# Kernel optimization log

Measured on AMD Instinct MI355X. Metric: run time of the kernel, lower is better.

## Reference

```python
import jax, jax.numpy as jnp
import numpy as np

B, T, H, LATENT, COND = 256, 256, 512, 64, 6
IN0 = 3 + H + 4  # lstm layer-0 input size


def _ln(x, g, b, eps=1e-5):
    m = x.mean(-1, keepdims=True)
    v = ((x - m) ** 2).mean(-1, keepdims=True)
    return (x - m) / jnp.sqrt(v + eps) * g + b


def setup_inputs() -> dict:
    key = jax.random.key(0)
    ks = jax.random.split(key, 24)
    p = lambda k, shape: (jax.random.normal(k, shape) * 0.02).astype(jnp.float32)
    inp = {
        'start': jax.random.uniform(ks[0], (B, 2), dtype=jnp.float32),
        'end': jax.random.uniform(ks[1], (B, 2), dtype=jnp.float32),
        'z': jax.random.normal(ks[2], (B, LATENT), dtype=jnp.float32),
        # condition encoder: Linear(6+latent->H), LN, Linear(H->H), LN
        'ce_w1': p(ks[3], (H, COND + LATENT)), 'ce_b1': jnp.zeros((H,), jnp.float32),
        'ce_g1': jnp.ones((H,), jnp.float32), 'ce_be1': jnp.zeros((H,), jnp.float32),
        'ce_w2': p(ks[4], (H, H)), 'ce_b2': jnp.zeros((H,), jnp.float32),
        'ce_g2': jnp.ones((H,), jnp.float32), 'ce_be2': jnp.zeros((H,), jnp.float32),
        # 2-layer LSTM (torch gate order i,f,g,o)
        'Wih0': p(ks[5], (4 * H, IN0)), 'Whh0': p(ks[6], (4 * H, H)),
        'bih0': jnp.zeros((4 * H,), jnp.float32), 'bhh0': jnp.zeros((4 * H,), jnp.float32),
        'Wih1': p(ks[7], (4 * H, H)), 'Whh1': p(ks[8], (4 * H, H)),
        'bih1': jnp.zeros((4 * H,), jnp.float32), 'bhh1': jnp.zeros((4 * H,), jnp.float32),
        # output head: Linear(H->H//2), LeakyReLU, Linear(H//2->3)
        'ow1': p(ks[9], (H // 2, H)), 'ob1': jnp.zeros((H // 2,), jnp.float32),
        'ow2': p(ks[10], (3, H // 2)), 'ob2': jnp.zeros((3,), jnp.float32),
        'init_in': jnp.zeros((1, 1, 3), jnp.float32),
        'max_len': T,
    }
    return inp


def _cell(x, h, c, Wih, Whh, bih, bhh):
    g = x @ Wih.T + bih + h @ Whh.T + bhh
    i, f, gg, o = jnp.split(g, 4, axis=-1)
    c2 = jax.nn.sigmoid(f) * c + jax.nn.sigmoid(i) * jnp.tanh(gg)
    h2 = jax.nn.sigmoid(o) * jnp.tanh(c2)
    return h2, c2


def reference(start, end, z, ce_w1, ce_b1, ce_g1, ce_be1, ce_w2, ce_b2, ce_g2, ce_be2,
              Wih0, Whh0, bih0, bhh0, Wih1, Whh1, bih1, bhh1,
              ow1, ob1, ow2, ob2, init_in, max_len):
    b = start.shape[0]
    hd = Whh0.shape[1]
    # condition vector
    diff = end - start
    dist = jnp.sqrt((diff ** 2).sum(-1, keepdims=True) + 1e-8)
    ang = jnp.arctan2(diff[:, 1:2], diff[:, 0:1])
    ci = jnp.concatenate([start, end, dist, ang, z], axis=-1)
    x = jax.nn.leaky_relu(_ln(ci @ ce_w1.T + ce_b1, ce_g1, ce_be1), 0.2)
    cond = jax.nn.leaky_relu(_ln(x @ ce_w2.T + ce_b2, ce_g2, ce_be2), 0.2)

    h0 = jnp.zeros((2, b, hd), start.dtype)
    c0 = jnp.zeros((2, b, hd), start.dtype)
    cur_in0 = jnp.broadcast_to(init_in.reshape(1, 3), (b, 3))

    def step(carry, _):
        h, c, cur_in, pos = carry
        rem = end - pos
        rd = jnp.sqrt((rem ** 2).sum(-1, keepdims=True) + 1e-8)
        ra = jnp.arctan2(rem[:, 1:2], rem[:, 0:1])
        xin = jnp.concatenate([cur_in, cond, rem, rd, ra], axis=-1)  # (B, 3+H+4)
        h1, c1 = _cell(xin, h[0], c[0], Wih0, Whh0, bih0, bhh0)
        h2, c2 = _cell(h1, h[1], c[1], Wih1, Whh1, bih1, bhh1)
        o = jax.nn.leaky_relu(h2 @ ow1.T + ob1, 0.2) @ ow2.T + ob2  # (B, 3)
        out = jnp.concatenate([o[:, :2], jax.nn.softplus(o[:, 2:3]) + 0.001], axis=-1)
        pos = pos + out[:, :2]
        return (jnp.stack([h1, h2]), jnp.stack([c1, c2]), out, pos), out

    _, outs = jax.lax.scan(step, (h0, c0, cur_in0, start), None, length=max_len)
    outputs = jnp.transpose(outs, (1, 0, 2))  # (B, T, 3)
    lengths = jnp.full((b,), max_len, dtype=jnp.int32)
    return outputs, lengths
```

## Files before the change

kernel.cpp:

```cpp
#include <hip/hip_runtime.h>
#include <math.h>

#define BB 256
#define TT 256
#define HH 512
#define G4 2048
#define IN0_ 519

typedef __bf16 bf16x8 __attribute__((ext_vector_type(8)));
typedef float  f32x4  __attribute__((ext_vector_type(4)));

__device__ __forceinline__ float sigf(float x) { return 1.0f / (1.0f + expf(-x)); }
__device__ __forceinline__ float leaky(float x) { return x > 0.f ? x : 0.2f * x; }

__device__ __forceinline__ unsigned short f2b(float x) {
    union { float f; unsigned int u; } v; v.f = x;
    unsigned int r = v.u + 0x7fffu + ((v.u >> 16) & 1u);
    return (unsigned short)(r >> 16);
}

__device__ __forceinline__ float block_sum(float v, float* red, int tid) {
    red[tid] = v; __syncthreads();
    for (int s = 128; s > 0; s >>= 1) {
        if (tid < s) red[tid] += red[tid + s];
        __syncthreads();
    }
    float r = red[0];
    __syncthreads();
    return r;
}

__global__ __launch_bounds__(256) void prep_weights(
    const float* __restrict__ Whh0, const float* __restrict__ Wih1,
    const float* __restrict__ Whh1, const float* __restrict__ Wih0,
    unsigned short* __restrict__ w0b, unsigned short* __restrict__ w1b,
    unsigned short* __restrict__ w2b, float* __restrict__ Wf)
{
    int idx = blockIdx.x * 256 + threadIdx.x;
    if (idx < G4 * HH) {
        w0b[idx] = f2b(Whh0[idx]);
        w1b[idx] = f2b(Wih1[idx]);
        w2b[idx] = f2b(Whh1[idx]);
    }
    if (idx < G4) {
        const int fc[7] = {0, 1, 2, 515, 516, 517, 518};
        #pragma unroll
        for (int f = 0; f < 7; f++) Wf[idx*8 + f] = Wih0[(size_t)idx*IN0_ + fc[f]];
        Wf[idx*8 + 7] = 0.f;
    }
}

__global__ void init_kernel(const float* __restrict__ start,
                            const float* __restrict__ init_in,
                            const int* __restrict__ max_len,
                            float* __restrict__ c0, float* __restrict__ c1,
                            unsigned short* __restrict__ h0u, unsigned short* __restrict__ h1u,
                            float* __restrict__ pos, float* __restrict__ cur,
                            float* __restrict__ out_tail)
{
    int i = blockIdx.x * blockDim.x + threadIdx.x;
    if (i < BB * HH) { c0[i] = 0.f; c1[i] = 0.f; h0u[i] = 0; h1u[i] = 0; }
    if (i < BB * 2) pos[i] = start[i];
    if (i < BB * 3) cur[i] = init_in[i % 3];
    if (i < BB)     out_tail[i] = (float)max_len[0];
}

__global__ __launch_bounds__(256) void cond_encoder(
    const float* __restrict__ start, const float* __restrict__ end,
    const float* __restrict__ z,
    const float* __restrict__ w1, const float* __restrict__ b1,
    const float* __restrict__ g1, const float* __restrict__ be1,
    const float* __restrict__ w2, const float* __restrict__ b2,
    const float* __restrict__ g2, const float* __restrict__ be2,
    float* __restrict__ cond)
{
    __shared__ float ci[70];
    __shared__ float xr[512];
    __shared__ float red[256];
    int b = blockIdx.x, tid = threadIdx.x;
    if (tid == 0) {
        float sx = start[2*b], sy = start[2*b+1];
        float ex = end[2*b],   ey = end[2*b+1];
        float dx = ex - sx, dy = ey - sy;
        ci[0]=sx; ci[1]=sy; ci[2]=ex; ci[3]=ey;
        ci[4]=sqrtf(dx*dx + dy*dy + 1e-8f);
        ci[5]=atan2f(dy, dx);
    }
    if (tid < 64) ci[6+tid] = z[b*64 + tid];
    __syncthreads();

    float pre0 = b1[tid], pre1 = b1[tid+256];
    {
        const float* r0 = w1 + (size_t)tid*70;
        const float* r1 = w1 + (size_t)(tid+256)*70;
        for (int k = 0; k < 70; k++) { float c = ci[k]; pre0 += c*r0[k]; pre1 += c*r1[k]; }
    }
    float m = block_sum(pre0+pre1, red, tid) * (1.f/512.f);
    float d0 = pre0-m, d1 = pre1-m;
    float v = block_sum(d0*d0 + d1*d1, red, tid) * (1.f/512.f);
    float rstd = rsqrtf(v + 1e-5f);
    xr[tid]     = leaky(d0*rstd*g1[tid]     + be1[tid]);
    xr[tid+256] = leaky(d1*rstd*g1[tid+256] + be1[tid+256]);
    __syncthreads();

    float q0 = b2[tid], q1 = b2[tid+256];
    {
        const float4* r0 = (const float4*)(w2 + (size_t)tid*512);
        const float4* r1 = (const float4*)(w2 + (size_t)(tid+256)*512);
        const float4* xv4 = (const float4*)xr;
        for (int q = 0; q < 128; q++) {
            float4 xv = xv4[q];
            float4 wa = r0[q], wb = r1[q];
            q0 += xv.x*wa.x + xv.y*wa.y + xv.z*wa.z + xv.w*wa.w;
            q1 += xv.x*wb.x + xv.y*wb.y + xv.z*wb.z + xv.w*wb.w;
        }
    }
    m = block_sum(q0+q1, red, tid) * (1.f/512.f);
    d0 = q0-m; d1 = q1-m;
    v = block_sum(d0*d0 + d1*d1, red, tid) * (1.f/512.f);
    rstd = rsqrtf(v + 1e-5f);
    cond[(size_t)b*512 + tid]     = leaky(d0*rstd*g2[tid]     + be2[tid]);
    cond[(size_t)b*512 + tid+256] = leaky(d1*rstd*g2[tid+256] + be2[tid+256]);
}

__global__ __launch_bounds__(256) void static_gates(
    const float* __restrict__ cond, const float* __restrict__ Wih0,
    const float* __restrict__ bih0, const float* __restrict__ bhh0,
    float* __restrict__ gs0)
{
    __shared__ float As[16][17];
    __shared__ float Bs[16][17];
    int tx = threadIdx.x & 15, ty = threadIdx.x >> 4;
    int brow = blockIdx.x * 16;
    int jcol = blockIdx.y * 16;
    float acc = 0.f;
    for (int kt = 0; kt < 512; kt += 16) {
        As[ty][tx] = cond[(size_t)(brow+ty)*512 + kt + tx];
        Bs[ty][tx] = Wih0[(size_t)(jcol+ty)*IN0_ + 3 + kt + tx];
        __syncthreads();
        #pragma unroll
        for (int kk = 0; kk < 16; kk++) acc += As[ty][kk] * Bs[tx][kk];
        __syncthreads();
    }
    int jg = jcol + tx;
    gs0[(size_t)(brow+ty)*G4 + jg] = acc + bih0[jg] + bhh0[jg];
}

__global__ __launch_bounds__(256) void lstm0_mfma(
    const unsigned short* __restrict__ Wb,
    const float* __restrict__ gs0,
    const float* __restrict__ Wf,
    const float* __restrict__ end, const float* __restrict__ pos,
    const float* __restrict__ cur,
    const unsigned short* __restrict__ h_in,
    const float* __restrict__ c_in,
    float* __restrict__ c_out,
    unsigned short* __restrict__ h_out)
{
    __shared__ float ct[4][16][16];
    __shared__ float feats[16][8];
    int tid = threadIdx.x;
    int w = tid >> 6, l = tid & 63;
    int lr = l & 15, lk = l >> 4;
    int m0 = blockIdx.x * 16;
    int n0 = blockIdx.y * 16;
    if (tid < 16) {
        int b = m0 + tid;
        float px = pos[2*b], py = pos[2*b+1];
        float ex = end[2*b], ey = end[2*b+1];
        float rx = ex - px, ry = ey - py;
        feats[tid][0] = cur[3*b];
        feats[tid][1] = cur[3*b+1];
        feats[tid][2] = cur[3*b+2];
        feats[tid][3] = rx;
        feats[tid][4] = ry;
        feats[tid][5] = sqrtf(rx*rx + ry*ry + 1e-8f);
        feats[tid][6] = atan2f(ry, rx);
        feats[tid][7] = 0.f;
    }
    int jg = w*512 + n0 + lr;
    f32x4 acc;
    #pragma unroll
    for (int r = 0; r < 4; r++)
        acc[r] = gs0[(size_t)(m0 + lk*4 + r)*G4 + jg];
    const unsigned short* ap = h_in + (size_t)(m0 + lr)*HH + lk*8;
    const unsigned short* bp = Wb   + (size_t)jg*HH + lk*8;
    #pragma unroll
    for (int kt = 0; kt < 16; kt++) {
        bf16x8 a = *reinterpret_cast<const bf16x8*>(ap + kt*32);
        bf16x8 b = *reinterpret_cast<const bf16x8*>(bp + kt*32);
        acc = __builtin_amdgcn_mfma_f32_16x16x32_bf16(a, b, acc, 0, 0, 0);
    }
    #pragma unroll
    for (int r = 0; r < 4; r++) ct[w][lk*4 + r][lr] = acc[r];
    __syncthreads();

    int bl = tid >> 4, jl = tid & 15;
    int b = m0 + bl;
    int j = n0 + jl;
    float g4[4];
    #pragma unroll
    for (int g = 0; g < 4; g++) {
        float v = ct[g][bl][jl];
        const float* wf = Wf + (size_t)(g*HH + j)*8;
        #pragma unroll
        for (int f = 0; f < 7; f++) v += feats[bl][f] * wf[f];
        g4[g] = v;
    }
    float ig = sigf(g4[0]), fg = sigf(g4[1]);
    float gg = tanhf(g4[2]), og = sigf(g4[3]);
    float cn = fg * c_in[(size_t)b*HH + j] + ig * gg;
    c_out[(size_t)b*HH + j] = cn;
    h_out[(size_t)b*HH + j] = f2b(og * tanhf(cn));
}

__global__ __launch_bounds__(256) void lstm1_mfma(
    const unsigned short* __restrict__ Wi,
    const unsigned short* __restrict__ Wh,
    const float* __restrict__ bi, const float* __restrict__ bh,
    const unsigned short* __restrict__ x,
    const unsigned short* __restrict__ h_in,
    const float* __restrict__ c_in,
    float* __restrict__ c_out,
    unsigned short* __restrict__ h_out, float* __restrict__ h_out_f)
{
    __shared__ float ct[4][16][16];
    int tid = threadIdx.x;
    int w = tid >> 6, l = tid & 63;
    int lr = l & 15, lk = l >> 4;
    int m0 = blockIdx.x * 16;
    int n0 = blockIdx.y * 16;
    int jg = w*512 + n0 + lr;
    float bs = bi[jg] + bh[jg];
    f32x4 acc;
    #pragma unroll
    for (int r = 0; r < 4; r++) acc[r] = bs;
    {
        const unsigned short* ap = x  + (size_t)(m0 + lr)*HH + lk*8;
        const unsigned short* bp = Wi + (size_t)jg*HH + lk*8;
        #pragma unroll
        for (int kt = 0; kt < 16; kt++) {
            bf16x8 a = *reinterpret_cast<const bf16x8*>(ap + kt*32);
            bf16x8 b = *reinterpret_cast<const bf16x8*>(bp + kt*32);
            acc = __builtin_amdgcn_mfma_f32_16x16x32_bf16(a, b, acc, 0, 0, 0);
        }
    }
    {
        const unsigned short* ap = h_in + (size_t)(m0 + lr)*HH + lk*8;
        const unsigned short* bp = Wh   + (size_t)jg*HH + lk*8;
        #pragma unroll
        for (int kt = 0; kt < 16; kt++) {
            bf16x8 a = *reinterpret_cast<const bf16x8*>(ap + kt*32);
            bf16x8 b = *reinterpret_cast<const bf16x8*>(bp + kt*32);
            acc = __builtin_amdgcn_mfma_f32_16x16x32_bf16(a, b, acc, 0, 0, 0);
        }
    }
    #pragma unroll
    for (int r = 0; r < 4; r++) ct[w][lk*4 + r][lr] = acc[r];
    __syncthreads();

    int bl = tid >> 4, jl = tid & 15;
    int b = m0 + bl;
    int j = n0 + jl;
    float ig = sigf(ct[0][bl][jl]), fg = sigf(ct[1][bl][jl]);
    float gg = tanhf(ct[2][bl][jl]), og = sigf(ct[3][bl][jl]);
    float cn = fg * c_in[(size_t)b*HH + j] + ig * gg;
    c_out[(size_t)b*HH + j] = cn;
    float hv = og * tanhf(cn);
    h_out[(size_t)b*HH + j] = f2b(hv);
    h_out_f[(size_t)b*HH + j] = hv;
}

__global__ __launch_bounds__(256) void head_kernel(
    const float* __restrict__ h2,
    const float* __restrict__ ow1, const float* __restrict__ ob1,
    const float* __restrict__ ow2, const float* __restrict__ ob2,
    float* __restrict__ outputs, float* __restrict__ pos, float* __restrict__ cur,
    int t)
{
    __shared__ float h2s[4][512];
    __shared__ float hid[4][256];
    __shared__ float osh[4][3];
    int tid = threadIdx.x;
    int b0 = blockIdx.x * 4;
    #pragma unroll
    for (int r = 0; r < 8; r++) {
        int idx = tid + r*256;
        int bi = idx >> 9, k = idx & 511;
        h2s[bi][k] = h2[(size_t)(b0+bi)*HH + k];
    }
    __syncthreads();
    float acc0 = ob1[tid], acc1 = acc0, acc2 = acc0, acc3 = acc0;
    {
        const float4* w4 = (const float4*)(ow1 + (size_t)tid*512);
        #pragma unroll 4
        for (int q = 0; q < 128; q++) {
            float4 w = w4[q];
            float4 a0 = *(const float4*)&h2s[0][q*4];
            float4 a1 = *(const float4*)&h2s[1][q*4];
            float4 a2 = *(const float4*)&h2s[2][q*4];
            float4 a3 = *(const float4*)&h2s[3][q*4];
            acc0 += a0.x*w.x + a0.y*w.y + a0.z*w.z + a0.w*w.w;
            acc1 += a1.x*w.x + a1.y*w.y + a1.z*w.z + a1.w*w.w;
            acc2 += a2.x*w.x + a2.y*w.y + a2.z*w.z + a2.w*w.w;
            acc3 += a3.x*w.x + a3.y*w.y + a3.z*w.z + a3.w*w.w;
        }
    }
    hid[0][tid] = leaky(acc0);
    hid[1][tid] = leaky(acc1);
    hid[2][tid] = leaky(acc2);
    hid[3][tid] = leaky(acc3);
    __syncthreads();
    int wave = tid >> 6, lane = tid & 63;
    #pragma unroll
    for (int r = 0; r < 3; r++) {
        float p = 0.f;
        #pragma unroll
        for (int q = 0; q < 4; q++) {
            int k = lane + q*64;
            p += hid[wave][k] * ow2[r*256 + k];
        }
        for (int off = 32; off; off >>= 1) p += __shfl_down(p, off);
        if (lane == 0) osh[wave][r] = p + ob2[r];
    }
    __syncthreads();
    if (tid < 4) {
        int b = b0 + tid;
        float o0 = osh[tid][0], o1 = osh[tid][1], o2 = osh[tid][2];
        float sp = (o2 > 20.f ? o2 : log1pf(expf(o2))) + 0.001f;
        float* op = outputs + ((size_t)b*TT + t)*3;
        op[0] = o0; op[1] = o1; op[2] = sp;
        pos[2*b]   += o0;
        pos[2*b+1] += o1;
        cur[3*b] = o0; cur[3*b+1] = o1; cur[3*b+2] = sp;
    }
}

extern "C" void kernel_launch(void* const* d_in, const int* in_sizes, int n_in,
                              void* d_out, int out_size, void* d_ws, size_t ws_size,
                              hipStream_t stream)
{
    const float* start  = (const float*)d_in[0];
    const float* end    = (const float*)d_in[1];
    const float* z      = (const float*)d_in[2];
    const float* ce_w1  = (const float*)d_in[3];
    const float* ce_b1  = (const float*)d_in[4];
    const float* ce_g1  = (const float*)d_in[5];
    const float* ce_be1 = (const float*)d_in[6];
    const float* ce_w2  = (const float*)d_in[7];
    const float* ce_b2  = (const float*)d_in[8];
    const float* ce_g2  = (const float*)d_in[9];
    const float* ce_be2 = (const float*)d_in[10];
    const float* Wih0   = (const float*)d_in[11];
    const float* Whh0   = (const float*)d_in[12];
    const float* bih0   = (const float*)d_in[13];
    const float* bhh0   = (const float*)d_in[14];
    const float* Wih1   = (const float*)d_in[15];
    const float* Whh1   = (const float*)d_in[16];
    const float* bih1   = (const float*)d_in[17];
    const float* bhh1   = (const float*)d_in[18];
    const float* ow1    = (const float*)d_in[19];
    const float* ob1    = (const float*)d_in[20];
    const float* ow2    = (const float*)d_in[21];
    const float* ob2    = (const float*)d_in[22];
    const float* init_in= (const float*)d_in[23];
    const int*   max_len= (const int*)d_in[24];

    float* out = (float*)d_out;
    float* ws  = (float*)d_ws;
    size_t off = 0;
    float* cond = ws + off; off += (size_t)BB*HH;
    float* gs0  = ws + off; off += (size_t)BB*G4;
    float* c0b[2]; c0b[0] = ws + off; off += (size_t)BB*HH; c0b[1] = ws + off; off += (size_t)BB*HH;
    float* c1b[2]; c1b[0] = ws + off; off += (size_t)BB*HH; c1b[1] = ws + off; off += (size_t)BB*HH;
    float* h1f  = ws + off; off += (size_t)BB*HH;
    float* Wf   = ws + off; off += (size_t)G4*8;
    float* pos  = ws + off; off += 512;
    float* cur  = ws + off; off += 1024;
    unsigned short* h0u[2];
    h0u[0] = (unsigned short*)(ws + off); off += (size_t)BB*HH/2;
    h0u[1] = (unsigned short*)(ws + off); off += (size_t)BB*HH/2;
    unsigned short* h1u[2];
    h1u[0] = (unsigned short*)(ws + off); off += (size_t)BB*HH/2;
    h1u[1] = (unsigned short*)(ws + off); off += (size_t)BB*HH/2;
    unsigned short* w0b = (unsigned short*)(ws + off); off += (size_t)G4*HH/2;
    unsigned short* w1b = (unsigned short*)(ws + off); off += (size_t)G4*HH/2;
    unsigned short* w2b = (unsigned short*)(ws + off); off += (size_t)G4*HH/2;

    prep_weights<<<dim3((G4*HH + 255)/256), dim3(256), 0, stream>>>(
        Whh0, Wih1, Whh1, Wih0, w0b, w1b, w2b, Wf);
    init_kernel<<<dim3((BB*HH + 255)/256), dim3(256), 0, stream>>>(
        start, init_in, max_len, c0b[0], c1b[0], h0u[0], h1u[0], pos, cur,
        out + (size_t)BB*TT*3);
    cond_encoder<<<dim3(BB), dim3(256), 0, stream>>>(
        start, end, z, ce_w1, ce_b1, ce_g1, ce_be1, ce_w2, ce_b2, ce_g2, ce_be2, cond);
    static_gates<<<dim3(16, 128), dim3(256), 0, stream>>>(cond, Wih0, bih0, bhh0, gs0);

    for (int t = 0; t < TT; t++) {
        int p = t & 1, np = p ^ 1;
        lstm0_mfma<<<dim3(16, 32), dim3(256), 0, stream>>>(
            w0b, gs0, Wf, end, pos, cur, h0u[p], c0b[p], c0b[np], h0u[np]);
        lstm1_mfma<<<dim3(16, 32), dim3(256), 0, stream>>>(
            w1b, w2b, bih1, bhh1, h0u[np], h1u[p], c1b[p], c1b[np], h1u[np], h1f);
        head_kernel<<<dim3(64), dim3(256), 0, stream>>>(
            h1f, ow1, ob1, ow2, ob2, out, pos, cur, t);
    }
}
```

Before: 12.00 ms.

## Fuse per-timestep LSTM launches into one persistent rollout kernel with team barriers

Replaces the 768 per-timestep kernel launches with a single persistent kernel. Each group of 16 blocks owns a 16-row batch tile and synchronizes via global atomic team barriers. Cell states stay in registers, while the head MLP runs on MFMA and each block recomputes positions and features redundantly. Weights are pre-swizzled into an MFMA fragment layout, A tiles are staged in swizzled LDS, and the static gate GEMM moves to bf16 MFMA. The persistent design relies on all 256 blocks being co-resident and adds spin-wait barrier latency.

```diff
diff --git a/kernel.cpp b/kernel.cpp
--- a/kernel.cpp
+++ b/kernel.cpp
@@ -9,14 +9,15 @@
 
 typedef __bf16 bf16x8 __attribute__((ext_vector_type(8)));
 typedef float  f32x4  __attribute__((ext_vector_type(4)));
+typedef unsigned short ushort;
 
 __device__ __forceinline__ float sigf(float x) { return 1.0f / (1.0f + expf(-x)); }
 __device__ __forceinline__ float leaky(float x) { return x > 0.f ? x : 0.2f * x; }
 
-__device__ __forceinline__ unsigned short f2b(float x) {
+__device__ __forceinline__ ushort f2b(float x) {
     union { float f; unsigned int u; } v; v.f = x;
     unsigned int r = v.u + 0x7fffu + ((v.u >> 16) & 1u);
-    return (unsigned short)(r >> 16);
+    return (ushort)(r >> 16);
 }
 
 __device__ __forceinline__ float block_sum(float v, float* red, int tid) {
@@ -30,39 +31,72 @@
     return r;
 }
 
-__global__ __launch_bounds__(256) void prep_weights(
+#define SWZB(row, bo) ((bo) ^ (((((row) ^ ((bo) >> 6)) & 7)) << 4))
+#define LDA(Abuf, lr_, lk_, kt_) \
+    (*(const bf16x8*)&Abuf[((lr_) * 1024 + SWZB((lr_), (kt_)*64 + (lk_)*16)) >> 1])
+
+__device__ __forceinline__ void stageA(ushort* dst, const ushort* src, int m0, int tid) {
+    int row = tid >> 4;
+    int lanebo = (tid & 15) * 64;
+    const ushort* sp = src + (size_t)(m0 + row) * HH;
+    #pragma unroll
+    for (int j = 0; j < 4; j++) {
+        int b2 = lanebo + j * 16;
+        uint4 v = *(const uint4*)(sp + (b2 >> 1));
+        *(uint4*)&dst[((row * 1024) + SWZB(row, b2)) >> 1] = v;
+    }
+}
+
+__device__ __forceinline__ void team_barrier(unsigned* cnt, unsigned target) {
+    __syncthreads();
+    if (threadIdx.x == 0) {
+        __threadfence();
+        __hip_atomic_fetch_add(cnt, 1u, __ATOMIC_RELEASE, __HIP_MEMORY_SCOPE_AGENT);
+        while (__hip_atomic_load(cnt, __ATOMIC_ACQUIRE, __HIP_MEMORY_SCOPE_AGENT) < target)
+            __builtin_amdgcn_s_sleep(2);
+        __threadfence();
+    }
+    __syncthreads();
+}
+
+#define SHIDX(jgt, kt, l_) ((((size_t)(jgt) * 16 + (kt)) * 64 + (l_)) * 8)
+
+__global__ __launch_bounds__(256) void prep_all(
     const float* __restrict__ Whh0, const float* __restrict__ Wih1,
     const float* __restrict__ Whh1, const float* __restrict__ Wih0,
-    unsigned short* __restrict__ w0b, unsigned short* __restrict__ w1b,
-    unsigned short* __restrict__ w2b, float* __restrict__ Wf)
+    const float* __restrict__ ow1,
+    ushort* __restrict__ w0s, ushort* __restrict__ w1s,
+    ushort* __restrict__ w2s, ushort* __restrict__ wi0s,
+    ushort* __restrict__ ow1s, float* __restrict__ Wf)
 {
-    int idx = blockIdx.x * 256 + threadIdx.x;
-    if (idx < G4 * HH) {
-        w0b[idx] = f2b(Whh0[idx]);
-        w1b[idx] = f2b(Wih1[idx]);
-        w2b[idx] = f2b(Whh1[idx]);
-    }
-    if (idx < G4) {
+    size_t idx = (size_t)blockIdx.x * 256 + threadIdx.x;
+    const size_t M = 1u << 20;
+    if (idx < 4 * M) {
+        int m = (int)(idx >> 20);
+        unsigned i = (unsigned)(idx & (M - 1));
+        int e = i & 7, ll = (i >> 3) & 63, kt = (i >> 9) & 15, jgt = i >> 13;
+        int jg = jgt * 16 + (ll & 15);
+        int k  = kt * 32 + ((ll >> 4) << 3) + e;
+        float v;
+        if (m == 0)      v = Whh0[(size_t)jg * 512 + k];
+        else if (m == 1) v = Wih1[(size_t)jg * 512 + k];
+        else if (m == 2) v = Whh1[(size_t)jg * 512 + k];
+        else             v = Wih0[(size_t)jg * IN0_ + 3 + k];
+        ushort* dst = (m == 0) ? w0s : (m == 1) ? w1s : (m == 2) ? w2s : wi0s;
+        dst[i] = f2b(v);
+    } else if (idx < 4 * M + 131072) {
+        unsigned i = (unsigned)(idx - 4 * M);
+        int e = i & 7, ll = (i >> 3) & 63, kt = (i >> 9) & 15, jgt = i >> 13;
+        int jg = jgt * 16 + (ll & 15);
+        int k  = kt * 32 + ((ll >> 4) << 3) + e;
+        ow1s[i] = f2b(ow1[(size_t)jg * 512 + k]);
+    } else if (idx < 4 * M + 131072 + 2048) {
+        int jrow = (int)(idx - (4 * M + 131072));
         const int fc[7] = {0, 1, 2, 515, 516, 517, 518};
         #pragma unroll
-        for (int f = 0; f < 7; f++) Wf[idx*8 + f] = Wih0[(size_t)idx*IN0_ + fc[f]];
-        Wf[idx*8 + 7] = 0.f;
-    }
-}
-
-__global__ void init_kernel(const float* __restrict__ start,
-                            const float* __restrict__ init_in,
-                            const int* __restrict__ max_len,
-                            float* __restrict__ c0, float* __restrict__ c1,
-                            unsigned short* __restrict__ h0u, unsigned short* __restrict__ h1u,
-                            float* __restrict__ pos, float* __restrict__ cur,
-                            float* __restrict__ out_tail)
-{
-    int i = blockIdx.x * blockDim.x + threadIdx.x;
-    if (i < BB * HH) { c0[i] = 0.f; c1[i] = 0.f; h0u[i] = 0; h1u[i] = 0; }
-    if (i < BB * 2) pos[i] = start[i];
-    if (i < BB * 3) cur[i] = init_in[i % 3];
-    if (i < BB)     out_tail[i] = (float)max_len[0];
+        for (int f = 0; f < 7; f++) Wf[jrow * 8 + f] = Wih0[(size_t)jrow * IN0_ + fc[f]];
+        Wf[jrow * 8 + 7] = 0.f;
+    }
 }
 
 __global__ __launch_bounds__(256) void cond_encoder(
@@ -72,7 +106,7 @@
     const float* __restrict__ g1, const float* __restrict__ be1,
     const float* __restrict__ w2, const float* __restrict__ b2,
     const float* __restrict__ g2, const float* __restrict__ be2,
-    float* __restrict__ cond)
+    ushort* __restrict__ condb)
 {
     __shared__ float ci[70];
     __shared__ float xr[512];
@@ -119,220 +153,268 @@
     d0 = q0-m; d1 = q1-m;
     v = block_sum(d0*d0 + d1*d1, red, tid) * (1.f/512.f);
     rstd = rsqrtf(v + 1e-5f);
-    cond[(size_t)b*512 + tid]     = leaky(d0*rstd*g2[tid]     + be2[tid]);
-    cond[(size_t)b*512 + tid+256] = leaky(d1*rstd*g2[tid+256] + be2[tid+256]);
-}
-
-__global__ __launch_bounds__(256) void static_gates(
-    const float* __restrict__ cond, const float* __restrict__ Wih0,
+    condb[(size_t)b*512 + tid]     = f2b(leaky(d0*rstd*g2[tid]     + be2[tid]));
+    condb[(size_t)b*512 + tid+256] = f2b(leaky(d1*rstd*g2[tid+256] + be2[tid+256]));
+}
+
+__global__ __launch_bounds__(256) void gs0_mfma(
+    const ushort* __restrict__ condb, const ushort* __restrict__ wi0s,
     const float* __restrict__ bih0, const float* __restrict__ bhh0,
     float* __restrict__ gs0)
 {
-    __shared__ float As[16][17];
-    __shared__ float Bs[16][17];
-    int tx = threadIdx.x & 15, ty = threadIdx.x >> 4;
-    int brow = blockIdx.x * 16;
-    int jcol = blockIdx.y * 16;
-    float acc = 0.f;
-    for (int kt = 0; kt < 512; kt += 16) {
-        As[ty][tx] = cond[(size_t)(brow+ty)*512 + kt + tx];
-        Bs[ty][tx] = Wih0[(size_t)(jcol+ty)*IN0_ + 3 + kt + tx];
-        __syncthreads();
-        #pragma unroll
-        for (int kk = 0; kk < 16; kk++) acc += As[ty][kk] * Bs[tx][kk];
-        __syncthreads();
-    }
-    int jg = jcol + tx;
-    gs0[(size_t)(brow+ty)*G4 + jg] = acc + bih0[jg] + bhh0[jg];
-}
-
-__global__ __launch_bounds__(256) void lstm0_mfma(
-    const unsigned short* __restrict__ Wb,
-    const float* __restrict__ gs0,
-    const float* __restrict__ Wf,
-    const float* __restrict__ end, const float* __restrict__ pos,
-    const float* __restrict__ cur,
-    const unsigned short* __restrict__ h_in,
-    const float* __restrict__ c_in,
-    float* __restrict__ c_out,
-    unsigned short* __restrict__ h_out)
+    __shared__ ushort A1[16*512];
+    int tid = threadIdx.x;
+    int bt = blockIdx.x >> 4, ct2 = blockIdx.x & 15;
+    int m0 = bt*16, hc0 = ct2*32;
+    int wid = tid >> 6, l = tid & 63, lr = l & 15, lk = l >> 4;
+    stageA(A1, condb, m0, tid);
+    __syncthreads();
+    int jgb = wid*512 + hc0;
+    float bv0 = bih0[jgb+lr]    + bhh0[jgb+lr];
+    float bv1 = bih0[jgb+16+lr] + bhh0[jgb+16+lr];
+    f32x4 a0, a1;
+    #pragma unroll
+    for (int r = 0; r < 4; r++) { a0[r] = bv0; a1[r] = bv1; }
+    int jgt = jgb >> 4;
+    #pragma unroll
+    for (int kt = 0; kt < 16; kt++) {
+        bf16x8 av = LDA(A1, lr, lk, kt);
+        bf16x8 b0 = *(const bf16x8*)&wi0s[SHIDX(jgt,   kt, l)];
+        bf16x8 b1 = *(const bf16x8*)&wi0s[SHIDX(jgt+1, kt, l)];
+        a0 = __builtin_amdgcn_mfma_f32_16x16x32_bf16(av, b0, a0, 0, 0, 0);
+        a1 = __builtin_amdgcn_mfma_f32_16x16x32_bf16(av, b1, a1, 0, 0, 0);
+    }
+    #pragma unroll
+    for (int r = 0; r < 4; r++) {
+        gs0[(size_t)(m0 + lk*4 + r)*G4 + jgb + lr]      = a0[r];
+        gs0[(size_t)(m0 + lk*4 + r)*G4 + jgb + 16 + lr] = a1[r];
+    }
+}
+
+__global__ __launch_bounds__(256, 1) void rollout(
+    const ushort* __restrict__ w0s, const ushort* __restrict__ w1s,
+    const ushort* __restrict__ w2s, const ushort* __restrict__ ow1s,
+    const float* __restrict__ gs0, const float* __restrict__ WfG,
+    const float* __restrict__ bih1, const float* __restrict__ bhh1,
+    const float* __restrict__ ob1, const float* __restrict__ ow2,
+    const float* __restrict__ ob2,
+    const float* __restrict__ start, const float* __restrict__ endp,
+    const float* __restrict__ init_in, const int* __restrict__ max_len,
+    ushort* __restrict__ h0A, ushort* __restrict__ h0B,
+    ushort* __restrict__ h1A, ushort* __restrict__ h1B,
+    float* __restrict__ outp, unsigned* __restrict__ bar)
 {
-    __shared__ float ct[4][16][16];
+    __shared__ ushort A1[16*512];
+    __shared__ ushort A2[16*512];
+    __shared__ float scratch[16*257];
+    __shared__ float WfS[4*32*9];
+    __shared__ ushort hstage[512];
     __shared__ float feats[16][8];
+    __shared__ float posS[16][2], endS[16][2], osumS[16][3];
+
     int tid = threadIdx.x;
-    int w = tid >> 6, l = tid & 63;
-    int lr = l & 15, lk = l >> 4;
-    int m0 = blockIdx.x * 16;
-    int n0 = blockIdx.y * 16;
+    int blk = blockIdx.x;
+    int xcd = blk & 7, wi = blk >> 3;
+    int ct = xcd*2 + (wi & 1);
+    int bt = wi >> 1;
+    int m0 = bt*16, hc0 = ct*32;
+    int wid = tid >> 6, l = tid & 63, lr = l & 15, lk = l >> 4;
+    unsigned* cnt = bar + bt*16;
+
+    for (int i = tid; i < 4*32*8; i += 256) {
+        int g = i >> 8, rem = i & 255, col = rem >> 3, f = rem & 7;
+        WfS[(g*32+col)*9 + f] = WfG[(size_t)(g*512 + hc0 + col)*8 + f];
+    }
     if (tid < 16) {
         int b = m0 + tid;
-        float px = pos[2*b], py = pos[2*b+1];
-        float ex = end[2*b], ey = end[2*b+1];
-        float rx = ex - px, ry = ey - py;
-        feats[tid][0] = cur[3*b];
-        feats[tid][1] = cur[3*b+1];
-        feats[tid][2] = cur[3*b+2];
-        feats[tid][3] = rx;
-        feats[tid][4] = ry;
-        feats[tid][5] = sqrtf(rx*rx + ry*ry + 1e-8f);
-        feats[tid][6] = atan2f(ry, rx);
-        feats[tid][7] = 0.f;
-    }
-    int jg = w*512 + n0 + lr;
-    f32x4 acc;
-    #pragma unroll
-    for (int r = 0; r < 4; r++)
-        acc[r] = gs0[(size_t)(m0 + lk*4 + r)*G4 + jg];
-    const unsigned short* ap = h_in + (size_t)(m0 + lr)*HH + lk*8;
-    const unsigned short* bp = Wb   + (size_t)jg*HH + lk*8;
-    #pragma unroll
-    for (int kt = 0; kt < 16; kt++) {
-        bf16x8 a = *reinterpret_cast<const bf16x8*>(ap + kt*32);
-        bf16x8 b = *reinterpret_cast<const bf16x8*>(bp + kt*32);
-        acc = __builtin_amdgcn_mfma_f32_16x16x32_bf16(a, b, acc, 0, 0, 0);
-    }
-    #pragma unroll
-    for (int r = 0; r < 4; r++) ct[w][lk*4 + r][lr] = acc[r];
-    __syncthreads();
-
-    int bl = tid >> 4, jl = tid & 15;
-    int b = m0 + bl;
-    int j = n0 + jl;
-    float g4[4];
-    #pragma unroll
-    for (int g = 0; g < 4; g++) {
-        float v = ct[g][bl][jl];
-        const float* wf = Wf + (size_t)(g*HH + j)*8;
+        posS[tid][0] = start[2*b]; posS[tid][1] = start[2*b+1];
+        endS[tid][0] = endp[2*b];  endS[tid][1] = endp[2*b+1];
+        if (ct == 0) outp[(size_t)BB*TT*3 + b] = (float)max_len[0];
+    }
+    __syncthreads();
+    if (tid < 16) {
+        float rx = endS[tid][0]-posS[tid][0], ry = endS[tid][1]-posS[tid][1];
+        feats[tid][0]=init_in[0]; feats[tid][1]=init_in[1]; feats[tid][2]=init_in[2];
+        feats[tid][3]=rx; feats[tid][4]=ry;
+        feats[tid][5]=sqrtf(rx*rx+ry*ry+1e-8f);
+        feats[tid][6]=atan2f(ry,rx);
+    }
+
+    f32x4 gsr[2]; float b1r[2]; float ob1r[4];
+    #pragma unroll
+    for (int nt = 0; nt < 2; nt++) {
+        int jg = wid*512 + hc0 + nt*16 + lr;
         #pragma unroll
-        for (int f = 0; f < 7; f++) v += feats[bl][f] * wf[f];
-        g4[g] = v;
-    }
-    float ig = sigf(g4[0]), fg = sigf(g4[1]);
-    float gg = tanhf(g4[2]), og = sigf(g4[3]);
-    float cn = fg * c_in[(size_t)b*HH + j] + ig * gg;
-    c_out[(size_t)b*HH + j] = cn;
-    h_out[(size_t)b*HH + j] = f2b(og * tanhf(cn));
-}
-
-__global__ __launch_bounds__(256) void lstm1_mfma(
-    const unsigned short* __restrict__ Wi,
-    const unsigned short* __restrict__ Wh,
-    const float* __restrict__ bi, const float* __restrict__ bh,
-    const unsigned short* __restrict__ x,
-    const unsigned short* __restrict__ h_in,
-    const float* __restrict__ c_in,
-    float* __restrict__ c_out,
-    unsigned short* __restrict__ h_out, float* __restrict__ h_out_f)
-{
-    __shared__ float ct[4][16][16];
-    int tid = threadIdx.x;
-    int w = tid >> 6, l = tid & 63;
-    int lr = l & 15, lk = l >> 4;
-    int m0 = blockIdx.x * 16;
-    int n0 = blockIdx.y * 16;
-    int jg = w*512 + n0 + lr;
-    float bs = bi[jg] + bh[jg];
-    f32x4 acc;
-    #pragma unroll
-    for (int r = 0; r < 4; r++) acc[r] = bs;
-    {
-        const unsigned short* ap = x  + (size_t)(m0 + lr)*HH + lk*8;
-        const unsigned short* bp = Wi + (size_t)jg*HH + lk*8;
+        for (int r = 0; r < 4; r++) gsr[nt][r] = gs0[(size_t)(m0 + lk*4 + r)*G4 + jg];
+        b1r[nt] = bih1[jg] + bhh1[jg];
+    }
+    #pragma unroll
+    for (int q = 0; q < 4; q++) ob1r[q] = ob1[wid*64 + q*16 + lr];
+
+    for (int i = tid; i < 512; i += 256) {
+        int row = i >> 5, col = i & 31;
+        h0A[(size_t)(m0+row)*HH + hc0 + col] = 0;
+        h1A[(size_t)(m0+row)*HH + hc0 + col] = 0;
+    }
+    float c00 = 0.f, c01 = 0.f, c10 = 0.f, c11 = 0.f;
+
+    unsigned bseq = 1;
+    team_barrier(cnt, bseq*16u);
+
+    int jgt0 = wid*32 + ct*2;
+    #pragma unroll 1
+    for (int t = 0; t < TT; t++) {
+        const ushort* h0in  = (t & 1) ? h0B : h0A;
+        ushort*       h0out = (t & 1) ? h0A : h0B;
+        const ushort* h1in  = (t & 1) ? h1B : h1A;
+        ushort*       h1out = (t & 1) ? h1A : h1B;
+
+        stageA(A1, h0in, m0, tid);
+        __syncthreads();
+        {
+            f32x4 a0 = gsr[0], a1 = gsr[1];
+            #pragma unroll
+            for (int kt = 0; kt < 16; kt++) {
+                bf16x8 av  = LDA(A1, lr, lk, kt);
+                bf16x8 b0  = *(const bf16x8*)&w0s[SHIDX(jgt0,   kt, l)];
+                bf16x8 b1v = *(const bf16x8*)&w0s[SHIDX(jgt0+1, kt, l)];
+                a0 = __builtin_amdgcn_mfma_f32_16x16x32_bf16(av, b0,  a0, 0, 0, 0);
+                a1 = __builtin_amdgcn_mfma_f32_16x16x32_bf16(av, b1v, a1, 0, 0, 0);
+            }
+            #pragma unroll
+            for (int r = 0; r < 4; r++) {
+                scratch[(wid*16 + lk*4 + r)*33 + lr]      = a0[r];
+                scratch[(wid*16 + lk*4 + r)*33 + 16 + lr] = a1[r];
+            }
+        }
+        __syncthreads();
         #pragma unroll
-        for (int kt = 0; kt < 16; kt++) {
-            bf16x8 a = *reinterpret_cast<const bf16x8*>(ap + kt*32);
-            bf16x8 b = *reinterpret_cast<const bf16x8*>(bp + kt*32);
-            acc = __builtin_amdgcn_mfma_f32_16x16x32_bf16(a, b, acc, 0, 0, 0);
-        }
-    }
-    {
-        const unsigned short* ap = h_in + (size_t)(m0 + lr)*HH + lk*8;
-        const unsigned short* bp = Wh   + (size_t)jg*HH + lk*8;
+        for (int s = 0; s < 2; s++) {
+            int cell = tid + s*256;
+            int row = cell >> 5, col = cell & 31;
+            float gv[4];
+            #pragma unroll
+            for (int g = 0; g < 4; g++) {
+                float v = scratch[(g*16 + row)*33 + col];
+                const float* wf = &WfS[(g*32 + col)*9];
+                #pragma unroll
+                for (int f = 0; f < 7; f++) v += feats[row][f] * wf[f];
+                gv[g] = v;
+            }
+            float cold = s ? c01 : c00;
+            float cn = sigf(gv[1])*cold + sigf(gv[0])*tanhf(gv[2]);
+            if (s) c01 = cn; else c00 = cn;
+            hstage[cell] = f2b(sigf(gv[3])*tanhf(cn));
+        }
+        __syncthreads();
+        if (tid < 64) {
+            int row = tid >> 2, cc = (tid & 3)*8;
+            *(uint4*)&h0out[(size_t)(m0+row)*HH + hc0 + cc] = *(const uint4*)&hstage[row*32 + cc];
+        }
+        bseq++; team_barrier(cnt, bseq*16u);
+
+        stageA(A1, h0out, m0, tid);
+        stageA(A2, h1in,  m0, tid);
+        __syncthreads();
+        {
+            f32x4 a0, a1;
+            #pragma unroll
+            for (int r = 0; r < 4; r++) { a0[r] = b1r[0]; a1[r] = b1r[1]; }
+            #pragma unroll
+            for (int kt = 0; kt < 16; kt++) {
+                bf16x8 av  = LDA(A1, lr, lk, kt);
+                bf16x8 b0  = *(const bf16x8*)&w1s[SHIDX(jgt0,   kt, l)];
+                bf16x8 b1v = *(const bf16x8*)&w1s[SHIDX(jgt0+1, kt, l)];
+                a0 = __builtin_amdgcn_mfma_f32_16x16x32_bf16(av, b0,  a0, 0, 0, 0);
+                a1 = __builtin_amdgcn_mfma_f32_16x16x32_bf16(av, b1v, a1, 0, 0, 0);
+            }
+            #pragma unroll
+            for (int kt = 0; kt < 16; kt++) {
+                bf16x8 av  = LDA(A2, lr, lk, kt);
+                bf16x8 b0  = *(const bf16x8*)&w2s[SHIDX(jgt0,   kt, l)];
+                bf16x8 b1v = *(const bf16x8*)&w2s[SHIDX(jgt0+1, kt, l)];
+                a0 = __builtin_amdgcn_mfma_f32_16x16x32_bf16(av, b0,  a0, 0, 0, 0);
+                a1 = __builtin_amdgcn_mfma_f32_16x16x32_bf16(av, b1v, a1, 0, 0, 0);
+            }
+            #pragma unroll
+            for (int r = 0; r < 4; r++) {
+                scratch[(wid*16 + lk*4 + r)*33 + lr]      = a0[r];
+                scratch[(wid*16 + lk*4 + r)*33 + 16 + lr] = a1[r];
+            }
+        }
+        __syncthreads();
         #pragma unroll
-        for (int kt = 0; kt < 16; kt++) {
-            bf16x8 a = *reinterpret_cast<const bf16x8*>(ap + kt*32);
-            bf16x8 b = *reinterpret_cast<const bf16x8*>(bp + kt*32);
-            acc = __builtin_amdgcn_mfma_f32_16x16x32_bf16(a, b, acc, 0, 0, 0);
-        }
-    }
-    #pragma unroll
-    for (int r = 0; r < 4; r++) ct[w][lk*4 + r][lr] = acc[r];
-    __syncthreads();
-
-    int bl = tid >> 4, jl = tid & 15;
-    int b = m0 + bl;
-    int j = n0 + jl;
-    float ig = sigf(ct[0][bl][jl]), fg = sigf(ct[1][bl][jl]);
-    float gg = tanhf(ct[2][bl][jl]), og = sigf(ct[3][bl][jl]);
-    float cn = fg * c_in[(size_t)b*HH + j] + ig * gg;
-    c_out[(size_t)b*HH + j] = cn;
-    float hv = og * tanhf(cn);
-    h_out[(size_t)b*HH + j] = f2b(hv);
-    h_out_f[(size_t)b*HH + j] = hv;
-}
-
-__global__ __launch_bounds__(256) void head_kernel(
-    const float* __restrict__ h2,
-    const float* __restrict__ ow1, const float* __restrict__ ob1,
-    const float* __restrict__ ow2, const float* __restrict__ ob2,
-    float* __restrict__ outputs, float* __restrict__ pos, float* __restrict__ cur,
-    int t)
-{
-    __shared__ float h2s[4][512];
-    __shared__ float hid[4][256];
-    __shared__ float osh[4][3];
-    int tid = threadIdx.x;
-    int b0 = blockIdx.x * 4;
-    #pragma unroll
-    for (int r = 0; r < 8; r++) {
-        int idx = tid + r*256;
-        int bi = idx >> 9, k = idx & 511;
-        h2s[bi][k] = h2[(size_t)(b0+bi)*HH + k];
-    }
-    __syncthreads();
-    float acc0 = ob1[tid], acc1 = acc0, acc2 = acc0, acc3 = acc0;
-    {
-        const float4* w4 = (const float4*)(ow1 + (size_t)tid*512);
-        #pragma unroll 4
-        for (int q = 0; q < 128; q++) {
-            float4 w = w4[q];
-            float4 a0 = *(const float4*)&h2s[0][q*4];
-            float4 a1 = *(const float4*)&h2s[1][q*4];
-            float4 a2 = *(const float4*)&h2s[2][q*4];
-            float4 a3 = *(const float4*)&h2s[3][q*4];
-            acc0 += a0.x*w.x + a0.y*w.y + a0.z*w.z + a0.w*w.w;
-            acc1 += a1.x*w.x + a1.y*w.y + a1.z*w.z + a1.w*w.w;
-            acc2 += a2.x*w.x + a2.y*w.y + a2.z*w.z + a2.w*w.w;
-            acc3 += a3.x*w.x + a3.y*w.y + a3.z*w.z + a3.w*w.w;
-        }
-    }
-    hid[0][tid] = leaky(acc0);
-    hid[1][tid] = leaky(acc1);
-    hid[2][tid] = leaky(acc2);
-    hid[3][tid] = leaky(acc3);
-    __syncthreads();
-    int wave = tid >> 6, lane = tid & 63;
-    #pragma unroll
-    for (int r = 0; r < 3; r++) {
-        float p = 0.f;
-        #pragma unroll
-        for (int q = 0; q < 4; q++) {
-            int k = lane + q*64;
-            p += hid[wave][k] * ow2[r*256 + k];
-        }
-        for (int off = 32; off; off >>= 1) p += __shfl_down(p, off);
-        if (lane == 0) osh[wave][r] = p + ob2[r];
-    }
-    __syncthreads();
-    if (tid < 4) {
-        int b = b0 + tid;
-        float o0 = osh[tid][0], o1 = osh[tid][1], o2 = osh[tid][2];
-        float sp = (o2 > 20.f ? o2 : log1pf(expf(o2))) + 0.001f;
-        float* op = outputs + ((size_t)b*TT + t)*3;
-        op[0] = o0; op[1] = o1; op[2] = sp;
-        pos[2*b]   += o0;
-        pos[2*b+1] += o1;
-        cur[3*b] = o0; cur[3*b+1] = o1; cur[3*b+2] = sp;
+        for (int s = 0; s < 2; s++) {
+            int cell = tid + s*256;
+            int row = cell >> 5, col = cell & 31;
+            float gi = scratch[(0*16+row)*33 + col];
+            float gf = scratch[(1*16+row)*33 + col];
+            float gg = scratch[(2*16+row)*33 + col];
+            float go = scratch[(3*16+row)*33 + col];
+            float cold = s ? c11 : c10;
+            float cn = sigf(gf)*cold + sigf(gi)*tanhf(gg);
+            if (s) c11 = cn; else c10 = cn;
+            hstage[cell] = f2b(sigf(go)*tanhf(cn));
+        }
+        __syncthreads();
+        if (tid < 64) {
+            int row = tid >> 2, cc = (tid & 3)*8;
+            *(uint4*)&h1out[(size_t)(m0+row)*HH + hc0 + cc] = *(const uint4*)&hstage[row*32 + cc];
+        }
+        bseq++; team_barrier(cnt, bseq*16u);
+
+        stageA(A1, h1out, m0, tid);
+        __syncthreads();
+        {
+            f32x4 hacc[4];
+            #pragma unroll
+            for (int q = 0; q < 4; q++) {
+                #pragma unroll
+                for (int r = 0; r < 4; r++) hacc[q][r] = ob1r[q];
+            }
+            #pragma unroll
+            for (int kt = 0; kt < 16; kt++) {
+                bf16x8 av = LDA(A1, lr, lk, kt);
+                #pragma unroll
+                for (int q = 0; q < 4; q++) {
+                    bf16x8 bv = *(const bf16x8*)&ow1s[SHIDX(wid*4 + q, kt, l)];
+                    hacc[q] = __builtin_amdgcn_mfma_f32_16x16x32_bf16(av, bv, hacc[q], 0, 0, 0);
+                }
+            }
+            #pragma unroll
+            for (int q = 0; q < 4; q++)
+                #pragma unroll
+                for (int r = 0; r < 4; r++)
+                    scratch[(lk*4 + r)*257 + wid*64 + q*16 + lr] = leaky(hacc[q][r]);
+        }
+        __syncthreads();
+        if (tid < 48) {
+            int row = tid & 15, rr = tid >> 4;
+            const float* w2r = ow2 + rr*256;
+            float sum = 0.f;
+            for (int kk = 0; kk < 256; kk++) {
+                int k = (kk + row*16) & 255;
+                sum += scratch[row*257 + k] * w2r[k];
+            }
+            osumS[row][rr] = sum + ob2[rr];
+        }
+        __syncthreads();
+        if (tid < 16) {
+            int row = tid;
+            float o0 = osumS[row][0], o1 = osumS[row][1], o2 = osumS[row][2];
+            float sp = (o2 > 20.f ? o2 : log1pf(expf(o2))) + 0.001f;
+            posS[row][0] += o0; posS[row][1] += o1;
+            if (ct == 0) {
+                float* op = outp + ((size_t)(m0+row)*TT + t)*3;
+                op[0] = o0; op[1] = o1; op[2] = sp;
+            }
+            float rx = endS[row][0]-posS[row][0], ry = endS[row][1]-posS[row][1];
+            feats[row][0]=o0; feats[row][1]=o1; feats[row][2]=sp;
+            feats[row][3]=rx; feats[row][4]=ry;
+            feats[row][5]=sqrtf(rx*rx+ry*ry+1e-8f);
+            feats[row][6]=atan2f(ry,rx);
+        }
+        __syncthreads();
     }
 }
 
@@ -369,40 +451,33 @@
     float* out = (float*)d_out;
     float* ws  = (float*)d_ws;
     size_t off = 0;
-    float* cond = ws + off; off += (size_t)BB*HH;
     float* gs0  = ws + off; off += (size_t)BB*G4;
-    float* c0b[2]; c0b[0] = ws + off; off += (size_t)BB*HH; c0b[1] = ws + off; off += (size_t)BB*HH;
-    float* c1b[2]; c1b[0] = ws + off; off += (size_t)BB*HH; c1b[1] = ws + off; off += (size_t)BB*HH;
-    float* h1f  = ws + off; off += (size_t)BB*HH;
-    float* Wf   = ws + off; off += (size_t)G4*8;
-    float* pos  = ws + off; off += 512;
-    float* cur  = ws + off; off += 1024;
-    unsigned short* h0u[2];
-    h0u[0] = (unsigned short*)(ws + off); off += (size_t)BB*HH/2;
-    h0u[1] = (unsigned short*)(ws + off); off += (size_t)BB*HH/2;
-    unsigned short* h1u[2];
-    h1u[0] = (unsigned short*)(ws + off); off += (size_t)BB*HH/2;
-    h1u[1] = (unsigned short*)(ws + off); off += (size_t)BB*HH/2;
-    unsigned short* w0b = (unsigned short*)(ws + off); off += (size_t)G4*HH/2;
-    unsigned short* w1b = (unsigned short*)(ws + off); off += (size_t)G4*HH/2;
-    unsigned short* w2b = (unsigned short*)(ws + off); off += (size_t)G4*HH/2;
-
-    prep_weights<<<dim3((G4*HH + 255)/256), dim3(256), 0, stream>>>(
-        Whh0, Wih1, Whh1, Wih0, w0b, w1b, w2b, Wf);
-    init_kernel<<<dim3((BB*HH + 255)/256), dim3(256), 0, stream>>>(
-        start, init_in, max_len, c0b[0], c1b[0], h0u[0], h1u[0], pos, cur,
-        out + (size_t)BB*TT*3);
+    float* WfG  = ws + off; off += (size_t)G4*8;
+    unsigned* bar = (unsigned*)(ws + off); off += 256;
+    ushort* us = (ushort*)(ws + off);
+    size_t uo = 0;
+    ushort* w0s  = us + uo; uo += (size_t)G4*HH;
+    ushort* w1s  = us + uo; uo += (size_t)G4*HH;
+    ushort* w2s  = us + uo; uo += (size_t)G4*HH;
+    ushort* wi0s = us + uo; uo += (size_t)G4*HH;
+    ushort* ow1s = us + uo; uo += (size_t)256*HH;
+    ushort* condb= us + uo; uo += (size_t)BB*HH;
+    ushort* h0A  = us + uo; uo += (size_t)BB*HH;
+    ushort* h0B  = us + uo; uo += (size_t)BB*HH;
+    ushort* h1A  = us + uo; uo += (size_t)BB*HH;
+    ushort* h1B  = us + uo; uo += (size_t)BB*HH;
+
+    hipMemsetAsync(bar, 0, 256*sizeof(unsigned), stream);
+    {
+        size_t total = (size_t)4*1048576 + 131072 + 2048;
+        prep_all<<<dim3((unsigned)((total + 255)/256)), dim3(256), 0, stream>>>(
+            Whh0, Wih1, Whh1, Wih0, ow1, w0s, w1s, w2s, wi0s, ow1s, WfG);
+    }
     cond_encoder<<<dim3(BB), dim3(256), 0, stream>>>(
-        start, end, z, ce_w1, ce_b1, ce_g1, ce_be1, ce_w2, ce_b2, ce_g2, ce_be2, cond);
-    static_gates<<<dim3(16, 128), dim3(256), 0, stream>>>(cond, Wih0, bih0, bhh0, gs0);
-
-    for (int t = 0; t < TT; t++) {
-        int p = t & 1, np = p ^ 1;
-        lstm0_mfma<<<dim3(16, 32), dim3(256), 0, stream>>>(
-            w0b, gs0, Wf, end, pos, cur, h0u[p], c0b[p], c0b[np], h0u[np]);
-        lstm1_mfma<<<dim3(16, 32), dim3(256), 0, stream>>>(
-            w1b, w2b, bih1, bhh1, h0u[np], h1u[p], c1b[p], c1b[np], h1u[np], h1f);
-        head_kernel<<<dim3(64), dim3(256), 0, stream>>>(
-            h1f, ow1, ob1, ow2, ob2, out, pos, cur, t);
-    }
-}
+        start, end, z, ce_w1, ce_b1, ce_g1, ce_be1, ce_w2, ce_b2, ce_g2, ce_be2, condb);
+    gs0_mfma<<<dim3(256), dim3(256), 0, stream>>>(condb, wi0s, bih0, bhh0, gs0);
+
+    rollout<<<dim3(256), dim3(256), 0, stream>>>(
+        w0s, w1s, w2s, ow1s, gs0, WfG, bih1, bhh1, ob1, ow2, ob2,
+        start, end, init_in, max_len, h0A, h0B, h1A, h1B, out, bar);
+}
```

Result: slower. 19.30 ms (+60.8%).
